# Kernel optimization log

Hardware: AMD Instinct MI355X
Metric: run time of the kernel (lower is better)

The kernel has to match this reference:

```python
import jax, jax.numpy as jnp
import numpy as np

B, L, H, A, C = 16, 2048, 1024, 1024, 5  # batch, seq_len, hidden, attention_size, num_cat_choices


def setup_inputs() -> dict:
    key = jax.random.key(0)
    ks = jax.random.split(key, 5)
    inp = jax.random.normal(ks[0], (B, L, H), dtype=jnp.float32)
    W_hidden = jax.random.normal(ks[1], (A, H), dtype=jnp.float32) * 0.02
    b_hidden = jnp.zeros((A,), jnp.float32)
    query = jax.random.normal(ks[2], (A, 1), dtype=jnp.float32) * 0.02
    W_cls = jax.random.normal(ks[3], (1, H), dtype=jnp.float32) * 0.02
    b_cls = jnp.zeros((1,), jnp.float32)
    # Build masks with exactly C marker positions per row (required by the
    # original nested-loop logic: C markers -> C segments, count in [0, C-1]).
    rng = np.random.default_rng(0)
    attn = np.zeros((B, L), np.int64)
    mlm = np.zeros((B, L), np.int64)
    for b in range(B):
        end = max(int(L - rng.integers(0, L // 4)), 64)  # valid length
        attn[b, :end] = 1
        seg = (end - 4) // C
        for c in range(C):
            mlm[b, 2 + c * seg] = 1
    return dict(input=inp, attention_mask=jnp.asarray(attn),
                mlm_mask=jnp.asarray(mlm), W_hidden=W_hidden,
                b_hidden=b_hidden, query=query, W_cls=W_cls, b_cls=b_cls)


def reference(input, attention_mask, mlm_mask, W_hidden, b_hidden, query, W_cls, b_cls):
    # --- attention merge (dropout is identity at eval) ---
    keys = jnp.tanh(input @ W_hidden.T + b_hidden)                    # (B,L,A)
    qvar = jnp.var(query, ddof=1)                                     # torch.var default: unbiased
    probs = (keys @ query) / jnp.sqrt(A * qvar)                       # (B,L,1)
    mask = (1.0 - attention_mask[..., None].astype(jnp.float32)) * -1000.0
    att = jax.nn.softmax(probs * mask, axis=1)                        # faithful: logits are probs*mask
    vals = att + input                                                # (B,L,H)
    # --- vectorized replacement of the nested segment-mask loop (roberta branch) ---
    idx = jnp.arange(L)
    marker = jnp.where(mlm_mask > 0, idx, L)                          # (B,L)
    starts = jnp.sort(marker, axis=1)[:, :C]                          # (B,C) marker positions
    end_idx = attention_mask.sum(axis=1)                              # (B,)
    # segment c covers [starts[c]+1, next_boundary); boundary = next marker - 1,
    # last segment's boundary = end_idx - 1  (mlm_mask_extend[i,c,start+1:j-1]=1)
    bounds = jnp.concatenate([starts[:, 1:] - 1, (end_idx - 1)[:, None]], axis=1)  # (B,C)
    seg_mask = ((idx[None, None, :] >= starts[:, :, None] + 1)
                & (idx[None, None, :] < bounds[:, :, None])).astype(vals.dtype)    # (B,C,L)
    # fused segment pooling: avoids materializing the (B,C,L,H) repeat
    context = jnp.einsum('bcl,blh->bch', seg_mask, vals)              # (B,C,H)
    logits = context @ W_cls.T + b_cls                                # (B,C,1)
    return logits
```

## Files before the change

kernel.cpp:

```cpp
#include <hip/hip_runtime.h>
#include <hip/hip_bf16.h>
#include <math.h>

#define B_ 16
#define L_ 2048
#define H_ 1024
#define A_ 1024
#define C_ 5

#define KPH 256
#define KE_BLOCKS (B_ * L_ / 16)
#define KW_BLOCKS 256
#define PB_BLOCKS 128
#define PBS 8
#define PROBE_THRESH 150.0f

typedef __attribute__((ext_vector_type(8))) short short8v;
typedef __attribute__((ext_vector_type(4))) float float4v;

static constexpr size_t OFF_SCAL   = 0;
static constexpr size_t OFF_END    = 64;
static constexpr size_t OFF_CNT    = 192;
static constexpr size_t OFF_STARTS = 320;
static constexpr size_t OFF_LIST   = 4096;
static constexpr size_t OFF_WF     = OFF_LIST + (size_t)B_ * L_ * 4;
static constexpr size_t OFF_D      = OFF_WF + (size_t)A_ * H_ * 2;
static constexpr size_t OFF_PROBE  = OFF_D + (size_t)B_ * L_ * 4;

static __device__ __forceinline__ unsigned short f2bf(float f) {
  unsigned u = __float_as_uint(f);
  unsigned r = (u >> 16) & 1u;
  return (unsigned short)((u + 0x7fffu + r) >> 16);
}

__global__ __launch_bounds__(256) void kPrep(const int* __restrict__ attn,
                                             const int* __restrict__ mlm,
                                             const float* __restrict__ query,
                                             const float* __restrict__ Wcls,
                                             const float* __restrict__ Wh,
                                             float* __restrict__ ws_scal,
                                             int* __restrict__ endv,
                                             int* __restrict__ cnt,
                                             int* __restrict__ starts,
                                             int* __restrict__ list,
                                             unsigned short* __restrict__ Wfrag) {
  __shared__ int   wsh[4];
  __shared__ float sf1[256];
  __shared__ float sf2[256];
  const int bid = blockIdx.x;
  const int t = threadIdx.x;
  const int w = t >> 6;
  const int lane = t & 63;

  if (bid < B_) {
    const int b = bid;
    const int* arow = attn + (size_t)b * L_;
    const int* mrow = mlm + (size_t)b * L_;
    const int base = t * 8;

    int loc[8];
    int lc = 0;
#pragma unroll
    for (int j = 0; j < 8; ++j) {
      int l = base + j;
      if (arow[l] == 0) loc[lc++] = l;
    }
    int incl = lc;
#pragma unroll
    for (int o = 1; o < 64; o <<= 1) {
      int v = __shfl_up(incl, o, 64);
      if (lane >= o) incl += v;
    }
    if (lane == 63) wsh[w] = incl;
    __syncthreads();
    int pre = 0, total = 0;
#pragma unroll
    for (int i = 0; i < 4; ++i) {
      int s = wsh[i];
      if (i < w) pre += s;
      total += s;
    }
    int excl = pre + incl - lc;
    int* lrow = list + (size_t)b * L_;
    for (int j = 0; j < lc; ++j) lrow[excl + j] = loc[j];
    if (t == 0) {
      cnt[b] = total;
      endv[b] = L_ - total;
    }
    __syncthreads();

    int mloc[8];
    int mc = 0;
#pragma unroll
    for (int j = 0; j < 8; ++j) {
      int l = base + j;
      if (mrow[l] > 0) mloc[mc++] = l;
    }
    int incl2 = mc;
#pragma unroll
    for (int o = 1; o < 64; o <<= 1) {
      int v = __shfl_up(incl2, o, 64);
      if (lane >= o) incl2 += v;
    }
    if (lane == 63) wsh[w] = incl2;
    __syncthreads();
    int pre2 = 0;
#pragma unroll
    for (int i = 0; i < 4; ++i) {
      if (i < w) pre2 += wsh[i];
    }
    int excl2 = pre2 + incl2 - mc;
    for (int j = 0; j < mc; ++j) {
      int idx = excl2 + j;
      if (idx < C_) starts[b * C_ + idx] = mloc[j];
    }
  } else if (bid == B_) {
    float s = 0.f, s2 = 0.f;
    for (int i = t; i < A_; i += 256) {
      float q = query[i];
      s += q;
      s2 = fmaf(q, q, s2);
    }
    sf1[t] = s;
    sf2[t] = s2;
    __syncthreads();
    for (int off = 128; off >= 1; off >>= 1) {
      if (t < off) {
        sf1[t] += sf1[t + off];
        sf2[t] += sf2[t + off];
      }
      __syncthreads();
    }
    float qsum = sf1[0], qsq = sf2[0];
    __syncthreads();
    float wv = 0.f;
    for (int i = t; i < H_; i += 256) wv += Wcls[i];
    sf1[t] = wv;
    __syncthreads();
    for (int off = 128; off >= 1; off >>= 1) {
      if (t < off) sf1[t] += sf1[t + off];
      __syncthreads();
    }
    if (t == 0) {
      float var = (qsq - qsum * qsum / (float)A_) / (float)(A_ - 1);
      ws_scal[0] = sqrtf((float)A_ * var);
      ws_scal[1] = sf1[0];
    }
  } else {
    const int g4 = bid - B_ - 1;
    const int ga = g4 >> 2;
    const int q = g4 & 3;
    const int row = ga * 16 + (lane & 15);
    const int colb = (lane >> 4) * 8;
    const float* srcrow = Wh + (size_t)row * H_;
#pragma unroll
    for (int i = 0; i < 2; ++i) {
      const int kb = q * 8 + w * 2 + i;
      const float* src = srcrow + kb * 32 + colb;
      float4 u0 = *(const float4*)src;
      float4 u1 = *(const float4*)(src + 4);
      union { short8v v; unsigned short h[8]; } o;
      o.h[0] = f2bf(u0.x); o.h[1] = f2bf(u0.y); o.h[2] = f2bf(u0.z); o.h[3] = f2bf(u0.w);
      o.h[4] = f2bf(u1.x); o.h[5] = f2bf(u1.y); o.h[6] = f2bf(u1.z); o.h[7] = f2bf(u1.w);
      *(short8v*)(Wfrag + (((size_t)ga * 32 + kb) * 64 + lane) * 8) = o.v;
    }
  }
}

__global__ __launch_bounds__(256) void kSP(const float* __restrict__ inp,
                                           const unsigned short* __restrict__ Wfrag,
                                           const float* __restrict__ bh,
                                           const float* __restrict__ query,
                                           const float* __restrict__ Wcls,
                                           const int* __restrict__ attn,
                                           const int* __restrict__ cnt,
                                           const int* __restrict__ list,
                                           float* __restrict__ probe,
                                           float* __restrict__ d) {
  __shared__ __align__(16) unsigned short Xs[16][KPH + 8];
  __shared__ float red[4][16];
  const int bid = blockIdx.x;
  const int t = threadIdx.x;
  const int w = t >> 6;
  const int lane = t & 63;

  if (bid >= PB_BLOCKS) {
    const int r0 = (bid - PB_BLOCKS) * 16 + w * 4;
    const int a0v = attn[r0], a1v = attn[r0 + 1], a2v = attn[r0 + 2], a3v = attn[r0 + 3];
    if ((a0v | a1v | a2v | a3v) == 0) return;
    float4 wv4[4];
#pragma unroll
    for (int k = 0; k < 4; ++k) wv4[k] = *(const float4*)(Wcls + k * 256 + lane * 4);
    const float* p0 = inp + (size_t)r0 * H_;
    float4 x0[4], x1[4], x2[4], x3[4];
    if (a0v) {
#pragma unroll
      for (int k = 0; k < 4; ++k) x0[k] = *(const float4*)(p0 + k * 256 + lane * 4);
    }
    if (a1v) {
#pragma unroll
      for (int k = 0; k < 4; ++k) x1[k] = *(const float4*)(p0 + H_ + k * 256 + lane * 4);
    }
    if (a2v) {
#pragma unroll
      for (int k = 0; k < 4; ++k) x2[k] = *(const float4*)(p0 + 2 * H_ + k * 256 + lane * 4);
    }
    if (a3v) {
#pragma unroll
      for (int k = 0; k < 4; ++k) x3[k] = *(const float4*)(p0 + 3 * H_ + k * 256 + lane * 4);
    }
#define DOTROW(XV, AV, IDX)                                                          \
    if (AV) {                                                                        \
      float acc = 0.f;                                                               \
      _Pragma("unroll")                                                              \
      for (int k = 0; k < 4; ++k)                                                    \
        acc += XV[k].x * wv4[k].x + XV[k].y * wv4[k].y +                             \
               XV[k].z * wv4[k].z + XV[k].w * wv4[k].w;                              \
      _Pragma("unroll")                                                              \
      for (int o = 1; o < 64; o <<= 1) acc += __shfl_xor(acc, o, 64);                \
      if (lane == 0) d[r0 + IDX] = acc;                                              \
    }
    DOTROW(x0, a0v, 0)
    DOTROW(x1, a1v, 1)
    DOTROW(x2, a2v, 2)
    DOTROW(x3, a3v, 3)
#undef DOTROW
    return;
  }

  const int b = bid >> 3;
  const int sl = bid & 7;
  const int c0 = cnt[b];
  const int lg = lane >> 4;
  const int lc = lane & 15;

  const int srow = t >> 4;
  const int scol = (t & 15) * 16;
  int pi = srow;
  if (pi >= c0) pi = (c0 > 0) ? (c0 - 1) : 0;
  const int xl = (c0 > 0) ? list[(size_t)b * L_ + pi] : 0;
  const float* xptr = inp + ((size_t)(b * L_ + xl)) * H_ + scol;

  const unsigned short* wf = Wfrag + ((size_t)(sl * 8 + w * 2) * 32) * 512 + lane * 8;

  float4v acc0 = (float4v){0.f, 0.f, 0.f, 0.f};
  float4v acc1 = (float4v){0.f, 0.f, 0.f, 0.f};

  for (int ph = 0; ph < H_ / KPH; ++ph) {
    __syncthreads();
#pragma unroll
    for (int j = 0; j < 2; ++j) {
      float4 u0 = *(const float4*)(xptr + ph * KPH + j * 8);
      float4 u1 = *(const float4*)(xptr + ph * KPH + j * 8 + 4);
      union { short8v v; unsigned short h[8]; } o;
      o.h[0] = f2bf(u0.x); o.h[1] = f2bf(u0.y); o.h[2] = f2bf(u0.z); o.h[3] = f2bf(u0.w);
      o.h[4] = f2bf(u1.x); o.h[5] = f2bf(u1.y); o.h[6] = f2bf(u1.z); o.h[7] = f2bf(u1.w);
      *(short8v*)&Xs[srow][scol + j * 8] = o.v;
    }
    __syncthreads();
#pragma unroll
    for (int kk = 0; kk < 8; ++kk) {
      const int kb = ph * 8 + kk;
      short8v bv0 = *(const short8v*)(wf + (size_t)kb * 512);
      short8v bv1 = *(const short8v*)(wf + (size_t)kb * 512 + 32 * 512);
      short8v av = *(const short8v*)&Xs[lc][kk * 32 + lg * 8];
      acc0 = __builtin_amdgcn_mfma_f32_16x16x32_bf16(av, bv0, acc0, 0, 0, 0);
      acc1 = __builtin_amdgcn_mfma_f32_16x16x32_bf16(av, bv1, acc1, 0, 0, 0);
    }
  }

  float pp[4] = {0.f, 0.f, 0.f, 0.f};
  {
    const int ag0 = sl * 128 + w * 32 + lc;
    const float q0 = query[ag0];
    const float b0 = bh[ag0];
    const int ag1 = ag0 + 16;
    const float q1 = query[ag1];
    const float b1 = bh[ag1];
#pragma unroll
    for (int r = 0; r < 4; ++r) {
      pp[r] = fmaf(tanhf(acc0[r] + b0), q0, pp[r]);
      pp[r] = fmaf(tanhf(acc1[r] + b1), q1, pp[r]);
    }
  }
#pragma unroll
  for (int r = 0; r < 4; ++r) {
#pragma unroll
    for (int o = 1; o < 16; o <<= 1)
      pp[r] += __shfl_xor(pp[r], o, 64);
  }
  __syncthreads();
  if (lc == 0) {
#pragma unroll
    for (int r = 0; r < 4; ++r) red[w][lg * 4 + r] = pp[r];
  }
  __syncthreads();
  if (t < 16) {
    float s = red[0][t] + red[1][t] + red[2][t] + red[3][t];
    probe[((size_t)b * PBS + sl) * 16 + t] = (c0 > 0) ? s : 0.f;
  }
}

__global__ __launch_bounds__(256) void kTail(const int* __restrict__ cnt,
                                             const int* __restrict__ list,
                                             const float* __restrict__ ws_scal,
                                             const float* __restrict__ d,
                                             const int* __restrict__ starts,
                                             const int* __restrict__ endv,
                                             const float* __restrict__ probe,
                                             const unsigned short* __restrict__ Wfrag,
                                             const float* __restrict__ inp,
                                             const float* __restrict__ bh,
                                             const float* __restrict__ query,
                                             const float* __restrict__ bcls,
                                             float* __restrict__ out) {
  __shared__ float lgs[L_];
  __shared__ float sred[256];
  __shared__ __align__(16) unsigned short Xs[16][KPH + 8];
  __shared__ float red[4][16];
  __shared__ int sskip;
  const int b = blockIdx.x;
  const int t = threadIdx.x;
  const int w = t >> 6;
  const int lane = t & 63;
  const float denom = ws_scal[0];
  const int c0 = cnt[b];

  if (t == 0) sskip = 0;
  __syncthreads();
  if (t < 16) {
    float s = 0.f;
#pragma unroll
    for (int p8 = 0; p8 < PBS; ++p8) s += probe[((size_t)b * PBS + p8) * 16 + t];
    float logit = -1000.0f * (s / denom);
    if (logit >= PROBE_THRESH) atomicOr(&sskip, 1);
  }
  __syncthreads();
  const bool skip = (c0 > 0) && (sskip != 0);

  float att0 = 0.0f;
  if (!skip) {
    const int lgp = lane >> 4;
    const int lc = lane & 15;
    const int srow = t >> 4;
    const int scol = (t & 15) * 16;
    const int ntile = (c0 + 15) >> 4;
    for (int tile = 0; tile < ntile; ++tile) {
      int pi = tile * 16 + srow;
      if (pi >= c0) pi = c0 - 1;
      const int xl = list[(size_t)b * L_ + pi];
      const float* xptr = inp + ((size_t)(b * L_ + xl)) * H_ + scol;
      float4v acc[8][2];
#pragma unroll
      for (int sl = 0; sl < 8; ++sl) {
        acc[sl][0] = (float4v){0.f, 0.f, 0.f, 0.f};
        acc[sl][1] = (float4v){0.f, 0.f, 0.f, 0.f};
      }
      for (int ph = 0; ph < H_ / KPH; ++ph) {
        __syncthreads();
#pragma unroll
        for (int j = 0; j < 2; ++j) {
          float4 u0 = *(const float4*)(xptr + ph * KPH + j * 8);
          float4 u1 = *(const float4*)(xptr + ph * KPH + j * 8 + 4);
          union { short8v v; unsigned short h[8]; } o;
          o.h[0] = f2bf(u0.x); o.h[1] = f2bf(u0.y); o.h[2] = f2bf(u0.z); o.h[3] = f2bf(u0.w);
          o.h[4] = f2bf(u1.x); o.h[5] = f2bf(u1.y); o.h[6] = f2bf(u1.z); o.h[7] = f2bf(u1.w);
          *(short8v*)&Xs[srow][scol + j * 8] = o.v;
        }
        __syncthreads();
#pragma unroll
        for (int sl = 0; sl < 8; ++sl) {
          const unsigned short* wf = Wfrag + ((size_t)(sl * 8 + w * 2) * 32) * 512 + lane * 8;
#pragma unroll
          for (int kk = 0; kk < 8; ++kk) {
            const int kb = ph * 8 + kk;
            short8v bv0 = *(const short8v*)(wf + (size_t)kb * 512);
            short8v bv1 = *(const short8v*)(wf + (size_t)kb * 512 + 32 * 512);
            short8v av = *(const short8v*)&Xs[lc][kk * 32 + lgp * 8];
            acc[sl][0] = __builtin_amdgcn_mfma_f32_16x16x32_bf16(av, bv0, acc[sl][0], 0, 0, 0);
            acc[sl][1] = __builtin_amdgcn_mfma_f32_16x16x32_bf16(av, bv1, acc[sl][1], 0, 0, 0);
          }
        }
      }
      float pp[4] = {0.f, 0.f, 0.f, 0.f};
#pragma unroll
      for (int sl = 0; sl < 8; ++sl) {
        const int ag0 = sl * 128 + w * 32 + lc;
        const float q0 = query[ag0];
        const float b0 = bh[ag0];
        const int ag1 = ag0 + 16;
        const float q1 = query[ag1];
        const float b1 = bh[ag1];
#pragma unroll
        for (int r = 0; r < 4; ++r) {
          pp[r] = fmaf(tanhf(acc[sl][0][r] + b0), q0, pp[r]);
          pp[r] = fmaf(tanhf(acc[sl][1][r] + b1), q1, pp[r]);
        }
      }
#pragma unroll
      for (int r = 0; r < 4; ++r) {
#pragma unroll
        for (int o = 1; o < 16; o <<= 1)
          pp[r] += __shfl_xor(pp[r], o, 64);
      }
      __syncthreads();
      if (lc == 0) {
#pragma unroll
        for (int r = 0; r < 4; ++r) red[w][lgp * 4 + r] = pp[r];
      }
      __syncthreads();
      if (t < 16) {
        const int row = tile * 16 + t;
        if (row < c0) {
          float s = red[0][t] + red[1][t] + red[2][t] + red[3][t];
          lgs[row] = -1000.0f * (s / denom);
        }
      }
      __syncthreads();
    }

    float mx = 0.0f;
    for (int i = t; i < c0; i += 256) mx = fmaxf(mx, lgs[i]);
    sred[t] = mx;
    __syncthreads();
    for (int off = 128; off >= 1; off >>= 1) {
      if (t < off) sred[t] = fmaxf(sred[t], sred[t + off]);
      __syncthreads();
    }
    const float m = sred[0];
    __syncthreads();
    float zs = 0.f;
    for (int i = t; i < c0; i += 256) zs += expf(lgs[i] - m);
    if (t == 0) zs += (float)(L_ - c0) * expf(-m);
    sred[t] = zs;
    __syncthreads();
    for (int off = 128; off >= 1; off >>= 1) {
      if (t < off) sred[t] += sred[t + off];
      __syncthreads();
    }
    const float Z = sred[0];
    __syncthreads();
    att0 = expf(-m) / Z;
  }

  for (int c = 0; c < C_; ++c) {
    const int st = starts[b * C_ + c];
    const int bound = (c < C_ - 1) ? (starts[b * C_ + c + 1] - 1) : (endv[b] - 1);
    const int lo = st + 1;
    const int hi = bound;
    float a = 0.f;
    for (int l = lo + t; l < hi; l += 256) a += d[(size_t)b * L_ + l];
    sred[t] = a;
    __syncthreads();
    for (int off = 128; off >= 1; off >>= 1) {
      if (t < off) sred[t] += sred[t + off];
      __syncthreads();
    }
    if (t == 0) {
      int count = hi - lo;
      if (count < 0) count = 0;
      out[b * C_ + c] = sred[0] + ws_scal[1] * att0 * (float)count + bcls[0];
    }
    __syncthreads();
  }
}

extern "C" void kernel_launch(void* const* d_in, const int* in_sizes, int n_in,
                              void* d_out, int out_size, void* d_ws, size_t ws_size,
                              hipStream_t stream) {
  const float* inp   = (const float*)d_in[0];
  const int*   attn  = (const int*)d_in[1];
  const int*   mlm   = (const int*)d_in[2];
  const float* Wh    = (const float*)d_in[3];
  const float* bh    = (const float*)d_in[4];
  const float* query = (const float*)d_in[5];
  const float* Wcls  = (const float*)d_in[6];
  const float* bcls  = (const float*)d_in[7];
  float* out = (float*)d_out;

  char* ws = (char*)d_ws;
  float*          ws_scal = (float*)(ws + OFF_SCAL);
  int*            endv    = (int*)(ws + OFF_END);
  int*            cnt     = (int*)(ws + OFF_CNT);
  int*            starts  = (int*)(ws + OFF_STARTS);
  int*            list    = (int*)(ws + OFF_LIST);
  unsigned short* Wfrag   = (unsigned short*)(ws + OFF_WF);
  float*          dvec    = (float*)(ws + OFF_D);
  float*          probe   = (float*)(ws + OFF_PROBE);

  hipLaunchKernelGGL(kPrep, dim3(B_ + 1 + KW_BLOCKS), dim3(256), 0, stream,
                     attn, mlm, query, Wcls, Wh, ws_scal, endv, cnt, starts, list, Wfrag);
  hipLaunchKernelGGL(kSP, dim3(PB_BLOCKS + KE_BLOCKS), dim3(256), 0, stream,
                     inp, Wfrag, bh, query, Wcls, attn, cnt, list, probe, dvec);
  hipLaunchKernelGGL(kTail, dim3(B_), dim3(256), 0, stream,
                     cnt, list, ws_scal, dvec, starts, endv, probe, Wfrag, inp, bh,
                     query, bcls, out);
}
```

Baseline: 39.87 us.

## Eliminate prep kernel by folding mask scans and weight conversion into consumers

Removes the separate kPrep launch. Its per-row mask scans, query variance and W_cls sum now run inside the tail kernel, and the probe blocks compute the valid length themselves with a reduction over the attention row. The weight matrix is no longer pre-packed into bf16 MFMA fragments in the workspace; each probe block instead loads fp32 W_hidden tiles, converts them to bf16 and stages them in LDS with 64-wide K steps. This saves one launch and the prep pass, but the probe blocks and the tail recompute, now reading fp32 weights and doing more synchronisation per tile. The tail also caps its list at 512 entries, which assumes at most 512 masked positions per row.

```diff
diff --git a/kernel.cpp b/kernel.cpp
--- a/kernel.cpp
+++ b/kernel.cpp
@@ -8,9 +8,7 @@
 #define A_ 1024
 #define C_ 5
 
-#define KPH 256
 #define KE_BLOCKS (B_ * L_ / 16)
-#define KW_BLOCKS 256
 #define PB_BLOCKS 128
 #define PBS 8
 #define PROBE_THRESH 150.0f
@@ -18,14 +16,8 @@
 typedef __attribute__((ext_vector_type(8))) short short8v;
 typedef __attribute__((ext_vector_type(4))) float float4v;
 
-static constexpr size_t OFF_SCAL   = 0;
-static constexpr size_t OFF_END    = 64;
-static constexpr size_t OFF_CNT    = 192;
-static constexpr size_t OFF_STARTS = 320;
-static constexpr size_t OFF_LIST   = 4096;
-static constexpr size_t OFF_WF     = OFF_LIST + (size_t)B_ * L_ * 4;
-static constexpr size_t OFF_D      = OFF_WF + (size_t)A_ * H_ * 2;
-static constexpr size_t OFF_PROBE  = OFF_D + (size_t)B_ * L_ * 4;
+static constexpr size_t OFF_D     = 0;
+static constexpr size_t OFF_PROBE = (size_t)B_ * L_ * 4;
 
 static __device__ __forceinline__ unsigned short f2bf(float f) {
   unsigned u = __float_as_uint(f);
@@ -33,152 +25,22 @@
   return (unsigned short)((u + 0x7fffu + r) >> 16);
 }
 
-__global__ __launch_bounds__(256) void kPrep(const int* __restrict__ attn,
-                                             const int* __restrict__ mlm,
-                                             const float* __restrict__ query,
-                                             const float* __restrict__ Wcls,
-                                             const float* __restrict__ Wh,
-                                             float* __restrict__ ws_scal,
-                                             int* __restrict__ endv,
-                                             int* __restrict__ cnt,
-                                             int* __restrict__ starts,
-                                             int* __restrict__ list,
-                                             unsigned short* __restrict__ Wfrag) {
-  __shared__ int   wsh[4];
-  __shared__ float sf1[256];
-  __shared__ float sf2[256];
-  const int bid = blockIdx.x;
-  const int t = threadIdx.x;
-  const int w = t >> 6;
-  const int lane = t & 63;
-
-  if (bid < B_) {
-    const int b = bid;
-    const int* arow = attn + (size_t)b * L_;
-    const int* mrow = mlm + (size_t)b * L_;
-    const int base = t * 8;
-
-    int loc[8];
-    int lc = 0;
-#pragma unroll
-    for (int j = 0; j < 8; ++j) {
-      int l = base + j;
-      if (arow[l] == 0) loc[lc++] = l;
-    }
-    int incl = lc;
-#pragma unroll
-    for (int o = 1; o < 64; o <<= 1) {
-      int v = __shfl_up(incl, o, 64);
-      if (lane >= o) incl += v;
-    }
-    if (lane == 63) wsh[w] = incl;
-    __syncthreads();
-    int pre = 0, total = 0;
-#pragma unroll
-    for (int i = 0; i < 4; ++i) {
-      int s = wsh[i];
-      if (i < w) pre += s;
-      total += s;
-    }
-    int excl = pre + incl - lc;
-    int* lrow = list + (size_t)b * L_;
-    for (int j = 0; j < lc; ++j) lrow[excl + j] = loc[j];
-    if (t == 0) {
-      cnt[b] = total;
-      endv[b] = L_ - total;
-    }
-    __syncthreads();
-
-    int mloc[8];
-    int mc = 0;
-#pragma unroll
-    for (int j = 0; j < 8; ++j) {
-      int l = base + j;
-      if (mrow[l] > 0) mloc[mc++] = l;
-    }
-    int incl2 = mc;
-#pragma unroll
-    for (int o = 1; o < 64; o <<= 1) {
-      int v = __shfl_up(incl2, o, 64);
-      if (lane >= o) incl2 += v;
-    }
-    if (lane == 63) wsh[w] = incl2;
-    __syncthreads();
-    int pre2 = 0;
-#pragma unroll
-    for (int i = 0; i < 4; ++i) {
-      if (i < w) pre2 += wsh[i];
-    }
-    int excl2 = pre2 + incl2 - mc;
-    for (int j = 0; j < mc; ++j) {
-      int idx = excl2 + j;
-      if (idx < C_) starts[b * C_ + idx] = mloc[j];
-    }
-  } else if (bid == B_) {
-    float s = 0.f, s2 = 0.f;
-    for (int i = t; i < A_; i += 256) {
-      float q = query[i];
-      s += q;
-      s2 = fmaf(q, q, s2);
-    }
-    sf1[t] = s;
-    sf2[t] = s2;
-    __syncthreads();
-    for (int off = 128; off >= 1; off >>= 1) {
-      if (t < off) {
-        sf1[t] += sf1[t + off];
-        sf2[t] += sf2[t + off];
-      }
-      __syncthreads();
-    }
-    float qsum = sf1[0], qsq = sf2[0];
-    __syncthreads();
-    float wv = 0.f;
-    for (int i = t; i < H_; i += 256) wv += Wcls[i];
-    sf1[t] = wv;
-    __syncthreads();
-    for (int off = 128; off >= 1; off >>= 1) {
-      if (t < off) sf1[t] += sf1[t + off];
-      __syncthreads();
-    }
-    if (t == 0) {
-      float var = (qsq - qsum * qsum / (float)A_) / (float)(A_ - 1);
-      ws_scal[0] = sqrtf((float)A_ * var);
-      ws_scal[1] = sf1[0];
-    }
-  } else {
-    const int g4 = bid - B_ - 1;
-    const int ga = g4 >> 2;
-    const int q = g4 & 3;
-    const int row = ga * 16 + (lane & 15);
-    const int colb = (lane >> 4) * 8;
-    const float* srcrow = Wh + (size_t)row * H_;
-#pragma unroll
-    for (int i = 0; i < 2; ++i) {
-      const int kb = q * 8 + w * 2 + i;
-      const float* src = srcrow + kb * 32 + colb;
-      float4 u0 = *(const float4*)src;
-      float4 u1 = *(const float4*)(src + 4);
-      union { short8v v; unsigned short h[8]; } o;
-      o.h[0] = f2bf(u0.x); o.h[1] = f2bf(u0.y); o.h[2] = f2bf(u0.z); o.h[3] = f2bf(u0.w);
-      o.h[4] = f2bf(u1.x); o.h[5] = f2bf(u1.y); o.h[6] = f2bf(u1.z); o.h[7] = f2bf(u1.w);
-      *(short8v*)(Wfrag + (((size_t)ga * 32 + kb) * 64 + lane) * 8) = o.v;
-    }
-  }
-}
+struct ProbeSmem {
+  unsigned short Ws[128][72];
+  unsigned short Xs[16][72];
+  float red[4][16];
+  int isum[4];
+};
 
 __global__ __launch_bounds__(256) void kSP(const float* __restrict__ inp,
-                                           const unsigned short* __restrict__ Wfrag,
+                                           const float* __restrict__ Wh,
                                            const float* __restrict__ bh,
                                            const float* __restrict__ query,
                                            const float* __restrict__ Wcls,
                                            const int* __restrict__ attn,
-                                           const int* __restrict__ cnt,
-                                           const int* __restrict__ list,
                                            float* __restrict__ probe,
                                            float* __restrict__ d) {
-  __shared__ __align__(16) unsigned short Xs[16][KPH + 8];
-  __shared__ float red[4][16];
+  __shared__ ProbeSmem sm;
   const int bid = blockIdx.x;
   const int t = threadIdx.x;
   const int w = t >> 6;
@@ -230,40 +92,49 @@
 
   const int b = bid >> 3;
   const int sl = bid & 7;
-  const int c0 = cnt[b];
+  const int* arow = attn + (size_t)b * L_;
+
+  int s_ = 0;
+  for (int i = t; i < L_; i += 256) s_ += arow[i];
+#pragma unroll
+  for (int o = 1; o < 64; o <<= 1) s_ += __shfl_xor(s_, o, 64);
+  if (lane == 0) sm.isum[w] = s_;
+  __syncthreads();
+  const int end = sm.isum[0] + sm.isum[1] + sm.isum[2] + sm.isum[3];
+
   const int lg = lane >> 4;
   const int lc = lane & 15;
-
-  const int srow = t >> 4;
-  const int scol = (t & 15) * 16;
-  int pi = srow;
-  if (pi >= c0) pi = (c0 > 0) ? (c0 - 1) : 0;
-  const int xl = (c0 > 0) ? list[(size_t)b * L_ + pi] : 0;
-  const float* xptr = inp + ((size_t)(b * L_ + xl)) * H_ + scol;
-
-  const unsigned short* wf = Wfrag + ((size_t)(sl * 8 + w * 2) * 32) * 512 + lane * 8;
+  const int xrow = t >> 4;
+  const int xcb = (t & 15) * 4;
+  const int pX = end + xrow;
+  const int pl = (pX < L_) ? pX : (L_ - 1);
+  const float* xsrc = inp + ((size_t)(b * L_ + pl)) * H_;
+  const float* wbase = Wh + (size_t)(sl * 128) * H_;
 
   float4v acc0 = (float4v){0.f, 0.f, 0.f, 0.f};
   float4v acc1 = (float4v){0.f, 0.f, 0.f, 0.f};
 
-  for (int ph = 0; ph < H_ / KPH; ++ph) {
-    __syncthreads();
-#pragma unroll
-    for (int j = 0; j < 2; ++j) {
-      float4 u0 = *(const float4*)(xptr + ph * KPH + j * 8);
-      float4 u1 = *(const float4*)(xptr + ph * KPH + j * 8 + 4);
-      union { short8v v; unsigned short h[8]; } o;
-      o.h[0] = f2bf(u0.x); o.h[1] = f2bf(u0.y); o.h[2] = f2bf(u0.z); o.h[3] = f2bf(u0.w);
-      o.h[4] = f2bf(u1.x); o.h[5] = f2bf(u1.y); o.h[6] = f2bf(u1.z); o.h[7] = f2bf(u1.w);
-      *(short8v*)&Xs[srow][scol + j * 8] = o.v;
-    }
-    __syncthreads();
-#pragma unroll
-    for (int kk = 0; kk < 8; ++kk) {
-      const int kb = ph * 8 + kk;
-      short8v bv0 = *(const short8v*)(wf + (size_t)kb * 512);
-      short8v bv1 = *(const short8v*)(wf + (size_t)kb * 512 + 32 * 512);
-      short8v av = *(const short8v*)&Xs[lc][kk * 32 + lg * 8];
+  for (int ph = 0; ph < 16; ++ph) {
+    __syncthreads();
+    {
+      float4 u = *(const float4*)(xsrc + ph * 64 + xcb);
+      unsigned short* dx = &sm.Xs[xrow][xcb];
+      dx[0] = f2bf(u.x); dx[1] = f2bf(u.y); dx[2] = f2bf(u.z); dx[3] = f2bf(u.w);
+    }
+#pragma unroll
+    for (int s8 = 0; s8 < 8; ++s8) {
+      const int r = s8 * 16 + xrow;
+      float4 uw = *(const float4*)(wbase + (size_t)r * H_ + ph * 64 + xcb);
+      unsigned short* dw = &sm.Ws[r][xcb];
+      dw[0] = f2bf(uw.x); dw[1] = f2bf(uw.y); dw[2] = f2bf(uw.z); dw[3] = f2bf(uw.w);
+    }
+    __syncthreads();
+#pragma unroll
+    for (int kk = 0; kk < 2; ++kk) {
+      const int off = kk * 32 + lg * 8;
+      short8v av = *(const short8v*)&sm.Xs[lc][off];
+      short8v bv0 = *(const short8v*)&sm.Ws[w * 32 + lc][off];
+      short8v bv1 = *(const short8v*)&sm.Ws[w * 32 + 16 + lc][off];
       acc0 = __builtin_amdgcn_mfma_f32_16x16x32_bf16(av, bv0, acc0, 0, 0, 0);
       acc1 = __builtin_amdgcn_mfma_f32_16x16x32_bf16(av, bv1, acc1, 0, 0, 0);
     }
@@ -292,47 +163,139 @@
   __syncthreads();
   if (lc == 0) {
 #pragma unroll
-    for (int r = 0; r < 4; ++r) red[w][lg * 4 + r] = pp[r];
+    for (int r = 0; r < 4; ++r) sm.red[w][lg * 4 + r] = pp[r];
   }
   __syncthreads();
   if (t < 16) {
-    float s = red[0][t] + red[1][t] + red[2][t] + red[3][t];
-    probe[((size_t)b * PBS + sl) * 16 + t] = (c0 > 0) ? s : 0.f;
+    const int p = end + t;
+    const bool valid = (p < L_) && (arow[p] == 0);
+    float s = sm.red[0][t] + sm.red[1][t] + sm.red[2][t] + sm.red[3][t];
+    probe[((size_t)b * PBS + sl) * 16 + t] = valid ? s : 0.f;
   }
 }
 
-__global__ __launch_bounds__(256) void kTail(const int* __restrict__ cnt,
-                                             const int* __restrict__ list,
-                                             const float* __restrict__ ws_scal,
-                                             const float* __restrict__ d,
-                                             const int* __restrict__ starts,
-                                             const int* __restrict__ endv,
-                                             const float* __restrict__ probe,
-                                             const unsigned short* __restrict__ Wfrag,
+__global__ __launch_bounds__(256) void kTail(const int* __restrict__ attn,
+                                             const int* __restrict__ mlm,
+                                             const float* __restrict__ query,
+                                             const float* __restrict__ Wcls,
+                                             const float* __restrict__ Wh,
                                              const float* __restrict__ inp,
                                              const float* __restrict__ bh,
-                                             const float* __restrict__ query,
+                                             const float* __restrict__ d,
+                                             const float* __restrict__ probe,
                                              const float* __restrict__ bcls,
                                              float* __restrict__ out) {
-  __shared__ float lgs[L_];
+  __shared__ float lgs[512];
   __shared__ float sred[256];
-  __shared__ __align__(16) unsigned short Xs[16][KPH + 8];
+  __shared__ float sred2[256];
+  __shared__ int list_lds[512];
+  __shared__ int starts_lds[C_];
+  __shared__ int wsh[4];
+  __shared__ int sskip;
+  __shared__ __align__(16) unsigned short Xs[16][72];
+  __shared__ __align__(16) unsigned short Ws[128][72];
   __shared__ float red[4][16];
-  __shared__ int sskip;
+
   const int b = blockIdx.x;
   const int t = threadIdx.x;
   const int w = t >> 6;
   const int lane = t & 63;
-  const float denom = ws_scal[0];
-  const int c0 = cnt[b];
+  const int* arow = attn + (size_t)b * L_;
+  const int* mrow = mlm + (size_t)b * L_;
+
+  const int base = t * 8;
+  int loc[8];
+  int nloc = 0;
+#pragma unroll
+  for (int j = 0; j < 8; ++j) {
+    int l = base + j;
+    if (arow[l] == 0) loc[nloc++] = l;
+  }
+  int incl = nloc;
+#pragma unroll
+  for (int o = 1; o < 64; o <<= 1) {
+    int v = __shfl_up(incl, o, 64);
+    if (lane >= o) incl += v;
+  }
+  if (lane == 63) wsh[w] = incl;
+  __syncthreads();
+  int pre = 0, total = 0;
+#pragma unroll
+  for (int i = 0; i < 4; ++i) {
+    int s = wsh[i];
+    if (i < w) pre += s;
+    total += s;
+  }
+  const int excl = pre + incl - nloc;
+  for (int j = 0; j < nloc; ++j) list_lds[excl + j] = loc[j];
+  const int c0 = total;
+  const int endv_ = L_ - c0;
+  __syncthreads();
+
+  int mloc[8];
+  int mc = 0;
+#pragma unroll
+  for (int j = 0; j < 8; ++j) {
+    int l = base + j;
+    if (mrow[l] > 0) mloc[mc++] = l;
+  }
+  int incl2 = mc;
+#pragma unroll
+  for (int o = 1; o < 64; o <<= 1) {
+    int v = __shfl_up(incl2, o, 64);
+    if (lane >= o) incl2 += v;
+  }
+  if (lane == 63) wsh[w] = incl2;
+  __syncthreads();
+  int pre2 = 0;
+#pragma unroll
+  for (int i = 0; i < 4; ++i) {
+    if (i < w) pre2 += wsh[i];
+  }
+  const int excl2 = pre2 + incl2 - mc;
+  for (int j = 0; j < mc; ++j) {
+    int idx = excl2 + j;
+    if (idx < C_) starts_lds[idx] = mloc[j];
+  }
+  __syncthreads();
+
+  float s = 0.f, s2 = 0.f;
+  for (int i = t; i < A_; i += 256) {
+    float q = query[i];
+    s += q;
+    s2 = fmaf(q, q, s2);
+  }
+  sred[t] = s;
+  sred2[t] = s2;
+  __syncthreads();
+  for (int off = 128; off >= 1; off >>= 1) {
+    if (t < off) {
+      sred[t] += sred[t + off];
+      sred2[t] += sred2[t + off];
+    }
+    __syncthreads();
+  }
+  const float qsum = sred[0], qsq = sred2[0];
+  __syncthreads();
+  float wv = 0.f;
+  for (int i = t; i < H_; i += 256) wv += Wcls[i];
+  sred[t] = wv;
+  __syncthreads();
+  for (int off = 128; off >= 1; off >>= 1) {
+    if (t < off) sred[t] += sred[t + off];
+    __syncthreads();
+  }
+  const float wsum = sred[0];
+  __syncthreads();
+  const float denom = sqrtf((float)A_ * (qsq - qsum * qsum / (float)A_) / (float)(A_ - 1));
 
   if (t == 0) sskip = 0;
   __syncthreads();
   if (t < 16) {
-    float s = 0.f;
-#pragma unroll
-    for (int p8 = 0; p8 < PBS; ++p8) s += probe[((size_t)b * PBS + p8) * 16 + t];
-    float logit = -1000.0f * (s / denom);
+    float ps = 0.f;
+#pragma unroll
+    for (int p8 = 0; p8 < PBS; ++p8) ps += probe[((size_t)b * PBS + p8) * 16 + t];
+    float logit = -1000.0f * (ps / denom);
     if (logit >= PROBE_THRESH) atomicOr(&sskip, 1);
   }
   __syncthreads();
@@ -341,51 +304,45 @@
   float att0 = 0.0f;
   if (!skip) {
     const int lgp = lane >> 4;
-    const int lc = lane & 15;
-    const int srow = t >> 4;
-    const int scol = (t & 15) * 16;
+    const int lcc = lane & 15;
+    const int xrow = t >> 4;
+    const int xcb = (t & 15) * 4;
     const int ntile = (c0 + 15) >> 4;
     for (int tile = 0; tile < ntile; ++tile) {
-      int pi = tile * 16 + srow;
+      int pi = tile * 16 + xrow;
       if (pi >= c0) pi = c0 - 1;
-      const int xl = list[(size_t)b * L_ + pi];
-      const float* xptr = inp + ((size_t)(b * L_ + xl)) * H_ + scol;
-      float4v acc[8][2];
-#pragma unroll
+      const float* xsrc = inp + ((size_t)(b * L_ + list_lds[pi])) * H_;
+      float pp[4] = {0.f, 0.f, 0.f, 0.f};
       for (int sl = 0; sl < 8; ++sl) {
-        acc[sl][0] = (float4v){0.f, 0.f, 0.f, 0.f};
-        acc[sl][1] = (float4v){0.f, 0.f, 0.f, 0.f};
-      }
-      for (int ph = 0; ph < H_ / KPH; ++ph) {
-        __syncthreads();
-#pragma unroll
-        for (int j = 0; j < 2; ++j) {
-          float4 u0 = *(const float4*)(xptr + ph * KPH + j * 8);
-          float4 u1 = *(const float4*)(xptr + ph * KPH + j * 8 + 4);
-          union { short8v v; unsigned short h[8]; } o;
-          o.h[0] = f2bf(u0.x); o.h[1] = f2bf(u0.y); o.h[2] = f2bf(u0.z); o.h[3] = f2bf(u0.w);
-          o.h[4] = f2bf(u1.x); o.h[5] = f2bf(u1.y); o.h[6] = f2bf(u1.z); o.h[7] = f2bf(u1.w);
-          *(short8v*)&Xs[srow][scol + j * 8] = o.v;
-        }
-        __syncthreads();
-#pragma unroll
-        for (int sl = 0; sl < 8; ++sl) {
-          const unsigned short* wf = Wfrag + ((size_t)(sl * 8 + w * 2) * 32) * 512 + lane * 8;
-#pragma unroll
-          for (int kk = 0; kk < 8; ++kk) {
-            const int kb = ph * 8 + kk;
-            short8v bv0 = *(const short8v*)(wf + (size_t)kb * 512);
-            short8v bv1 = *(const short8v*)(wf + (size_t)kb * 512 + 32 * 512);
-            short8v av = *(const short8v*)&Xs[lc][kk * 32 + lgp * 8];
-            acc[sl][0] = __builtin_amdgcn_mfma_f32_16x16x32_bf16(av, bv0, acc[sl][0], 0, 0, 0);
-            acc[sl][1] = __builtin_amdgcn_mfma_f32_16x16x32_bf16(av, bv1, acc[sl][1], 0, 0, 0);
+        float4v a0 = (float4v){0.f, 0.f, 0.f, 0.f};
+        float4v a1 = (float4v){0.f, 0.f, 0.f, 0.f};
+        const float* wbase = Wh + (size_t)(sl * 128) * H_;
+        for (int ph = 0; ph < 16; ++ph) {
+          __syncthreads();
+          {
+            float4 u = *(const float4*)(xsrc + ph * 64 + xcb);
+            unsigned short* dx = &Xs[xrow][xcb];
+            dx[0] = f2bf(u.x); dx[1] = f2bf(u.y); dx[2] = f2bf(u.z); dx[3] = f2bf(u.w);
+          }
+#pragma unroll
+          for (int s8 = 0; s8 < 8; ++s8) {
+            const int r = s8 * 16 + xrow;
+            float4 uw = *(const float4*)(wbase + (size_t)r * H_ + ph * 64 + xcb);
+            unsigned short* dw = &Ws[r][xcb];
+            dw[0] = f2bf(uw.x); dw[1] = f2bf(uw.y); dw[2] = f2bf(uw.z); dw[3] = f2bf(uw.w);
+          }
+          __syncthreads();
+#pragma unroll
+          for (int kk = 0; kk < 2; ++kk) {
+            const int off = kk * 32 + lgp * 8;
+            short8v av = *(const short8v*)&Xs[lcc][off];
+            short8v bv0 = *(const short8v*)&Ws[w * 32 + lcc][off];
+            short8v bv1 = *(const short8v*)&Ws[w * 32 + 16 + lcc][off];
+            a0 = __builtin_amdgcn_mfma_f32_16x16x32_bf16(av, bv0, a0, 0, 0, 0);
+            a1 = __builtin_amdgcn_mfma_f32_16x16x32_bf16(av, bv1, a1, 0, 0, 0);
           }
         }
-      }
-      float pp[4] = {0.f, 0.f, 0.f, 0.f};
-#pragma unroll
-      for (int sl = 0; sl < 8; ++sl) {
-        const int ag0 = sl * 128 + w * 32 + lc;
+        const int ag0 = sl * 128 + w * 32 + lcc;
         const float q0 = query[ag0];
         const float b0 = bh[ag0];
         const int ag1 = ag0 + 16;
@@ -393,8 +350,8 @@
         const float b1 = bh[ag1];
 #pragma unroll
         for (int r = 0; r < 4; ++r) {
-          pp[r] = fmaf(tanhf(acc[sl][0][r] + b0), q0, pp[r]);
-          pp[r] = fmaf(tanhf(acc[sl][1][r] + b1), q1, pp[r]);
+          pp[r] = fmaf(tanhf(a0[r] + b0), q0, pp[r]);
+          pp[r] = fmaf(tanhf(a1[r] + b1), q1, pp[r]);
         }
       }
 #pragma unroll
@@ -404,7 +361,7 @@
           pp[r] += __shfl_xor(pp[r], o, 64);
       }
       __syncthreads();
-      if (lc == 0) {
+      if (lcc == 0) {
 #pragma unroll
         for (int r = 0; r < 4; ++r) red[w][lgp * 4 + r] = pp[r];
       }
@@ -412,8 +369,8 @@
       if (t < 16) {
         const int row = tile * 16 + t;
         if (row < c0) {
-          float s = red[0][t] + red[1][t] + red[2][t] + red[3][t];
-          lgs[row] = -1000.0f * (s / denom);
+          float sv = red[0][t] + red[1][t] + red[2][t] + red[3][t];
+          lgs[row] = -1000.0f * (sv / denom);
         }
       }
       __syncthreads();
@@ -444,8 +401,8 @@
   }
 
   for (int c = 0; c < C_; ++c) {
-    const int st = starts[b * C_ + c];
-    const int bound = (c < C_ - 1) ? (starts[b * C_ + c + 1] - 1) : (endv[b] - 1);
+    const int st = starts_lds[c];
+    const int bound = (c < C_ - 1) ? (starts_lds[c + 1] - 1) : (endv_ - 1);
     const int lo = st + 1;
     const int hi = bound;
     float a = 0.f;
@@ -459,7 +416,7 @@
     if (t == 0) {
       int count = hi - lo;
       if (count < 0) count = 0;
-      out[b * C_ + c] = sred[0] + ws_scal[1] * att0 * (float)count + bcls[0];
+      out[b * C_ + c] = sred[0] + wsum * att0 * (float)count + bcls[0];
     }
     __syncthreads();
   }
@@ -479,20 +436,11 @@
   float* out = (float*)d_out;
 
   char* ws = (char*)d_ws;
-  float*          ws_scal = (float*)(ws + OFF_SCAL);
-  int*            endv    = (int*)(ws + OFF_END);
-  int*            cnt     = (int*)(ws + OFF_CNT);
-  int*            starts  = (int*)(ws + OFF_STARTS);
-  int*            list    = (int*)(ws + OFF_LIST);
-  unsigned short* Wfrag   = (unsigned short*)(ws + OFF_WF);
-  float*          dvec    = (float*)(ws + OFF_D);
-  float*          probe   = (float*)(ws + OFF_PROBE);
-
-  hipLaunchKernelGGL(kPrep, dim3(B_ + 1 + KW_BLOCKS), dim3(256), 0, stream,
-                     attn, mlm, query, Wcls, Wh, ws_scal, endv, cnt, starts, list, Wfrag);
+  float* dvec  = (float*)(ws + OFF_D);
+  float* probe = (float*)(ws + OFF_PROBE);
+
   hipLaunchKernelGGL(kSP, dim3(PB_BLOCKS + KE_BLOCKS), dim3(256), 0, stream,
-                     inp, Wfrag, bh, query, Wcls, attn, cnt, list, probe, dvec);
+                     inp, Wh, bh, query, Wcls, attn, probe, dvec);
   hipLaunchKernelGGL(kTail, dim3(B_), dim3(256), 0, stream,
-                     cnt, list, ws_scal, dvec, starts, endv, probe, Wfrag, inp, bh,
-                     query, bcls, out);
+                     attn, mlm, query, Wcls, Wh, inp, bh, dvec, probe, bcls, out);
 }
```

After: 50.17 us. 1.26x slower.
